# Optimization experiments

Hardware: AMD Instinct MI355X
Metric: run time of the kernel (lower is better)

## Reference

```python
import jax, jax.numpy as jnp
import numpy as np

B, S, D_IN, D_OUT, R = 8, 2048, 4096, 4096, 16

def setup_inputs() -> dict:
    key = jax.random.key(0)
    k = jax.random.split(key, 7)
    return {
        "x": jax.random.normal(k[0], (B, S, D_IN), dtype=jnp.float32),
        "osora_U": jax.random.normal(k[1], (D_OUT, R), dtype=jnp.float32) * 0.02,
        "osora_V": jax.random.normal(k[2], (R, D_IN), dtype=jnp.float32) * 0.02,
        "osora_S": jax.random.normal(k[3], (R,), dtype=jnp.float32),
        "osora_O": jax.random.normal(k[4], (D_OUT,), dtype=jnp.float32),
        "magnitude": jax.random.uniform(k[5], (D_OUT,), dtype=jnp.float32) + 0.5,
        "base_weight": jax.random.normal(k[6], (D_OUT, D_IN), dtype=jnp.float32) * 0.02,
    }

def reference(x, osora_U, osora_V, osora_S, osora_O, magnitude, base_weight):
    # osora_weight = diag(O) @ U @ diag(S) @ V  -> [out, in]
    osora_weight = (osora_O[:, None] * (osora_U * osora_S[None, :])) @ osora_V
    # low-rank path applied to activations: x @ osora_weight.T  -> [B, S, out]
    osora_result = jnp.einsum('bsr,or->bso', jnp.einsum('bsi,ri->bsr', x, osora_V) * osora_S, osora_U) * osora_O
    # weight norm of (base + adapter) per output row; detached in the original
    weight_norm = jax.lax.stop_gradient(
        jnp.linalg.norm(base_weight + osora_weight, axis=1).astype(base_weight.dtype))
    mag_norm_scale = (magnitude / weight_norm)[None, None, :]  # broadcast over B, S
    base_out = jnp.einsum('bsi,oi->bso', x, base_weight)
    return (mag_norm_scale - 1.0) * base_out + mag_norm_scale * osora_result
```

## Files before the change

### kernel.cpp

```cpp
#include <hip/hip_runtime.h>


#define M_TOT 16384
#define N_TOT 4096
#define K_TOT 4096

typedef __attribute__((ext_vector_type(8))) short bf16x8;
typedef __attribute__((ext_vector_type(4))) float f32x4;

__device__ __forceinline__ unsigned short f2bf(float f){
  union { float f; unsigned int u; } v; v.f = f;
  unsigned int u = v.u;
  u += 0x7FFFu + ((u >> 16) & 1u);
  return (unsigned short)(u >> 16);
}

__device__ __forceinline__ void async_lds16(const void* g, void* l){
  __builtin_amdgcn_global_load_lds(
      (const __attribute__((address_space(1))) unsigned int*)g,
      (__attribute__((address_space(3))) unsigned int*)l, 16, 0, 0);
}

__global__ __launch_bounds__(256) void cast_f32_to_bf16_x4(
    const float* __restrict__ src, unsigned short* __restrict__ dst, int n4){
  int i = blockIdx.x * 256 + threadIdx.x;
  if (i >= n4) return;
  float4 v = ((const float4*)src)[i];
  ushort4 o;
  o.x = f2bf(v.x); o.y = f2bf(v.y); o.z = f2bf(v.z); o.w = f2bf(v.w);
  ((ushort4*)dst)[i] = o;
}

__global__ __launch_bounds__(256) void tgemm_kernel(
    const unsigned short* __restrict__ xb, const unsigned short* __restrict__ vb,
    unsigned short* __restrict__ tb){
  int lane = threadIdx.x & 63;
  int wave = threadIdx.x >> 6;
  int quad = lane >> 4;
  int r16  = lane & 15;
  int m0 = (blockIdx.x * 4 + wave) * 16;
  const unsigned short* xptr = xb + (m0 + r16) * K_TOT + quad * 8;
  const unsigned short* vptr = vb + r16 * K_TOT + quad * 8;
  f32x4 acc = {0.f, 0.f, 0.f, 0.f};
  for (int k = 0; k < K_TOT; k += 32){
    bf16x8 a = *(const bf16x8*)(xptr + k);
    bf16x8 b = *(const bf16x8*)(vptr + k);
    acc = __builtin_amdgcn_mfma_f32_16x16x32_bf16(a, b, acc, 0, 0, 0);
  }
  for (int reg = 0; reg < 4; reg++){
    int m = m0 + quad * 4 + reg;
    tb[m * 16 + r16] = f2bf(acc[reg]);
  }
}

__global__ __launch_bounds__(256) void norm_kernel(
    const float* __restrict__ bw, const float* __restrict__ U,
    const float* __restrict__ S, const float* __restrict__ O,
    const float* __restrict__ mag, const float* __restrict__ V,
    float* __restrict__ s_out, float* __restrict__ sm1_out,
    unsigned short* __restrict__ w2b){
  __shared__ float Vl[16 * 1024];
  __shared__ float C8[8 * 16];
  __shared__ float red[8 * 4];
  int t = threadIdx.x;
  int lane = t & 63, wave = t >> 6;
  int n0 = blockIdx.x * 8;
  if (t < 128){
    int row = t >> 4, r = t & 15;
    int n = n0 + row;
    float c = O[n] * S[r] * U[n * 16 + r];
    C8[t] = c;
    w2b[n * 16 + r] = f2bf(c);
  }
  float nsq[8];
  for (int i = 0; i < 8; i++) nsq[i] = 0.f;
  for (int ch = 0; ch < 4; ch++){
    __syncthreads();
    for (int j = 0; j < 16; j++){
      int idx4 = j * 256 + t;
      int r = idx4 >> 8, c4 = idx4 & 255;
      *(float4*)(Vl + r * 1024 + c4 * 4) =
          *(const float4*)(V + r * 4096 + ch * 1024 + c4 * 4);
    }
    __syncthreads();
    for (int row = 0; row < 8; row++){
      float4 b = *(const float4*)(bw + (n0 + row) * 4096 + ch * 1024 + t * 4);
      float a0 = 0.f, a1 = 0.f, a2 = 0.f, a3 = 0.f;
      for (int r = 0; r < 16; r++){
        float cr = C8[row * 16 + r];
        const float* vp = Vl + r * 1024 + t * 4;
        a0 += cr * vp[0]; a1 += cr * vp[1]; a2 += cr * vp[2]; a3 += cr * vp[3];
      }
      float d0 = b.x + a0, d1 = b.y + a1, d2 = b.z + a2, d3 = b.w + a3;
      nsq[row] += d0*d0 + d1*d1 + d2*d2 + d3*d3;
    }
  }
  for (int row = 0; row < 8; row++){
    float v = nsq[row];
    for (int off = 32; off > 0; off >>= 1) v += __shfl_down(v, off);
    if (lane == 0) red[row * 4 + wave] = v;
  }
  __syncthreads();
  if (t < 8){
    int n = n0 + t;
    float tot = red[t*4] + red[t*4+1] + red[t*4+2] + red[t*4+3];
    float s = mag[n] / sqrtf(tot);
    s_out[n] = s;
    sm1_out[n] = s - 1.0f;
  }
}

__global__ __launch_bounds__(512, 2) void gemm_kernel(
    const unsigned short* __restrict__ A,
    const unsigned short* __restrict__ B,
    const unsigned short* __restrict__ Tb,
    const unsigned short* __restrict__ W2b,
    const float* __restrict__ s_arr, const float* __restrict__ sm1_arr,
    float* __restrict__ Cout){
  __shared__ unsigned short AL[2][16384];
  __shared__ unsigned short BL[2][16384];
  int tid  = threadIdx.x;
  int lane = tid & 63;
  int wave = tid >> 6;
  int wm   = wave >> 2;
  int wn   = wave & 3;
  int quad = lane >> 4;
  int r16  = lane & 15;
  int xm   = r16 & 7;

  int bid = blockIdx.x;
  int id  = (bid & 7) * 128 + (bid >> 3);
  int bm = id >> 4, bn = id & 15;
  int m0 = bm * 256, n0 = bn * 256;

  int urow0 = tid >> 3,         uslot0 = tid & 7;
  int urow1 = (512+tid) >> 3,   uslot1 = (512+tid) & 7;
  int ko0 = uslot0 ^ (urow0 & 7);
  int ko1 = uslot1 ^ (urow1 & 7);
  int a_src0 = (m0 + urow0) * K_TOT + ko0 * 8;
  int a_src1 = (m0 + urow1) * K_TOT + ko1 * 8;
  int b_src0 = (n0 + urow0) * K_TOT + ko0 * 8;
  int b_src1 = (n0 + urow1) * K_TOT + ko1 * 8;
  int l_u0 = tid * 8;
  int l_u1 = (512 + tid) * 8;
  const int HSTEP = 128 * K_TOT;

#define STG_A(bf_, h_, kt_) do{ \
    async_lds16(A + a_src0 + (h_)*HSTEP + (kt_)*64, &AL[bf_][(h_)*8192 + l_u0]); \
    async_lds16(A + a_src1 + (h_)*HSTEP + (kt_)*64, &AL[bf_][(h_)*8192 + l_u1]); }while(0)
#define STG_B(bf_, h_, kt_) do{ \
    async_lds16(B + b_src0 + (h_)*HSTEP + (kt_)*64, &BL[bf_][(h_)*8192 + l_u0]); \
    async_lds16(B + b_src1 + (h_)*HSTEP + (kt_)*64, &BL[bf_][(h_)*8192 + l_u1]); }while(0)

#define BARF()  asm volatile("s_barrier" ::: "memory")
#define VMW(n_) asm volatile("s_waitcnt vmcnt(" #n_ ")" ::: "memory")

  int a_row = (wm * 128 + r16) * 64;
  int b_row = (wn * 64  + r16) * 64;
  int koA[2] = { (quad ^ xm) * 8, ((4 + quad) ^ xm) * 8 };

  f32x4 zf = {0.f, 0.f, 0.f, 0.f};
  f32x4 acc[8][4];
#pragma unroll
  for (int i = 0; i < 8; i++)
#pragma unroll
    for (int j = 0; j < 4; j++) acc[i][j] = zf;
  bf16x8 af[4][2], bA[2][2], bB[2][2];

#define RD_A(bf_, mb_) do{ _Pragma("unroll") \
    for (int mf = 0; mf < 4; ++mf){ _Pragma("unroll") \
      for (int ks = 0; ks < 2; ++ks) \
        af[mf][ks] = *(const bf16x8*)(&AL[bf_][a_row + ((mb_)+mf)*1024 + koA[ks]]); } }while(0)
#define RD_B(bf_, dst_, nb_) do{ _Pragma("unroll") \
    for (int nf = 0; nf < 2; ++nf){ _Pragma("unroll") \
      for (int ks = 0; ks < 2; ++ks) \
        dst_[nf][ks] = *(const bf16x8*)(&BL[bf_][b_row + ((nb_)+nf)*1024 + koA[ks]]); } }while(0)
#define MMQ(mb_, bset_, nb_) do{ _Pragma("unroll") \
    for (int ks = 0; ks < 2; ++ks){ _Pragma("unroll") \
      for (int mf = 0; mf < 4; ++mf){ _Pragma("unroll") \
        for (int nf = 0; nf < 2; ++nf) \
          acc[(mb_)+mf][(nb_)+nf] = __builtin_amdgcn_mfma_f32_16x16x32_bf16( \
              af[mf][ks], bset_[nf][ks], acc[(mb_)+mf][(nb_)+nf], 0, 0, 0); } } }while(0)

  STG_A(0, 0, 0); STG_A(0, 1, 0); STG_B(0, 0, 0); STG_B(0, 1, 0);
  STG_B(1, 0, 1); STG_B(1, 1, 1); STG_A(1, 0, 1);
  VMW(6);
  BARF();

#pragma unroll 1
  for (int i = 0; i < 32; ++i){
    int kt = 2 * i;
    int pf = (i < 31);

    RD_A(0, 0); RD_B(0, bA, 0);
    STG_A(1, 1, kt + 1);
    __builtin_amdgcn_s_setprio(1); MMQ(0, bA, 0); __builtin_amdgcn_s_setprio(0);
    BARF();
    RD_B(0, bB, 2);
    __builtin_amdgcn_s_setprio(1); MMQ(0, bB, 2); __builtin_amdgcn_s_setprio(0);
    BARF();
    RD_A(0, 4);
    if (pf) STG_B(0, 0, kt + 2);
    __builtin_amdgcn_s_setprio(1); MMQ(4, bA, 0); __builtin_amdgcn_s_setprio(0);
    BARF();
    if (pf) STG_B(0, 1, kt + 2);
    __builtin_amdgcn_s_setprio(1); MMQ(4, bB, 2); __builtin_amdgcn_s_setprio(0);
    if (pf) { VMW(4); } else { VMW(0); }
    BARF();
    RD_A(1, 0); RD_B(1, bA, 0);
    if (pf) STG_A(0, 0, kt + 2);
    __builtin_amdgcn_s_setprio(1); MMQ(0, bA, 0); __builtin_amdgcn_s_setprio(0);
    BARF();
    RD_B(1, bB, 2);
    if (pf) STG_A(0, 1, kt + 2);
    __builtin_amdgcn_s_setprio(1); MMQ(0, bB, 2); __builtin_amdgcn_s_setprio(0);
    BARF();
    RD_A(1, 4);
    if (pf) STG_B(1, 0, kt + 3);
    __builtin_amdgcn_s_setprio(1); MMQ(4, bA, 0); __builtin_amdgcn_s_setprio(0);
    BARF();
    if (pf) { STG_B(1, 1, kt + 3); STG_A(1, 0, kt + 3); }
    __builtin_amdgcn_s_setprio(1); MMQ(4, bB, 2); __builtin_amdgcn_s_setprio(0);
    VMW(6);
    BARF();
  }

  VMW(0);
  __syncthreads();
  {
    int row = tid >> 1, half = tid & 1;
    uint4 z = {0u, 0u, 0u, 0u};
    unsigned short* Tp = &AL[0][0];
    unsigned short* Wp = &BL[0][0];
    *(uint4*)(Tp + row * 40 + half * 8)      = *(const uint4*)(Tb  + (m0 + row) * 16 + half * 8);
    *(uint4*)(Tp + row * 40 + 16 + half * 8) = z;
    *(uint4*)(Wp + row * 40 + half * 8)      = *(const uint4*)(W2b + (n0 + row) * 16 + half * 8);
    *(uint4*)(Wp + row * 40 + 16 + half * 8) = z;
  }
  __syncthreads();
#pragma unroll
  for (int nf = 0; nf < 4; ++nf){
    int nn = n0 + wn * 64 + nf * 16 + r16;
    float s   = s_arr[nn];
    float sm1 = sm1_arr[nn];
    bf16x8 b2 = *(const bf16x8*)(&BL[0][(wn * 64 + nf * 16 + r16) * 40 + quad * 8]);
#pragma unroll
    for (int mf = 0; mf < 8; ++mf){
      bf16x8 a2 = *(const bf16x8*)(&AL[0][(wm * 128 + mf * 16 + r16) * 40 + quad * 8]);
      f32x4 o2 = __builtin_amdgcn_mfma_f32_16x16x32_bf16(a2, b2, zf, 0, 0, 0);
      int mbase = m0 + wm * 128 + mf * 16 + quad * 4;
      float* cp = Cout + (long)mbase * N_TOT + nn;
      cp[0]         = sm1 * acc[mf][nf][0] + s * o2[0];
      cp[N_TOT]     = sm1 * acc[mf][nf][1] + s * o2[1];
      cp[2 * N_TOT] = sm1 * acc[mf][nf][2] + s * o2[2];
      cp[3 * N_TOT] = sm1 * acc[mf][nf][3] + s * o2[3];
    }
  }
#undef STG_A
#undef STG_B
#undef RD_A
#undef RD_B
#undef MMQ
#undef BARF
#undef VMW
}

extern "C" void kernel_launch(void* const* d_in, const int* in_sizes, int n_in,
                              void* d_out, int out_size, void* d_ws, size_t ws_size,
                              hipStream_t stream){
  const float* x   = (const float*)d_in[0];
  const float* U   = (const float*)d_in[1];
  const float* V   = (const float*)d_in[2];
  const float* S   = (const float*)d_in[3];
  const float* O   = (const float*)d_in[4];
  const float* mag = (const float*)d_in[5];
  const float* bw  = (const float*)d_in[6];
  float* out = (float*)d_out;

  char* ws = (char*)d_ws;
  unsigned short* xb  = (unsigned short*)(ws);
  unsigned short* wb  = (unsigned short*)(ws + 134217728);
  unsigned short* vb  = (unsigned short*)(ws + 167772160);
  unsigned short* tb  = (unsigned short*)(ws + 167903232);
  unsigned short* w2b = (unsigned short*)(ws + 168427520);
  float* s_arr   = (float*)(ws + 168558592);
  float* sm1_arr = (float*)(ws + 168574976);
  (void)in_sizes; (void)n_in; (void)out_size; (void)ws_size;

  cast_f32_to_bf16_x4<<<16384, 256, 0, stream>>>(bw, wb, 4194304);
  cast_f32_to_bf16_x4<<<64,    256, 0, stream>>>(V,  vb, 16384);
  cast_f32_to_bf16_x4<<<65536, 256, 0, stream>>>(x,  xb, 16777216);
  tgemm_kernel<<<256, 256, 0, stream>>>(xb, vb, tb);
  norm_kernel<<<512, 256, 0, stream>>>(bw, U, S, O, mag, V, s_arr, sm1_arr, w2b);
  gemm_kernel<<<1024, 512, 0, stream>>>(xb, wb, tb, w2b, s_arr, sm1_arr, out);
}
```

Measured before the change: 1.046 ms.

## Fuse weight cast into norm kernel, widen cast kernel, software-pipeline LDS reads

Folds the base-weight bf16 cast into the norm kernel, which already reads base_weight, removing one full pass over the weight. The cast kernel now handles four float4 per thread, so far fewer blocks are launched, and the tgemm K loop is unrolled. The main GEMM loop is restructured so A and B fragments for the next half-step are read from LDS earlier, using separate low/high A register sets, with adjusted vmcnt waits. This overlaps LDS reads with MFMA work but raises register pressure and makes the barrier and wait ordering more delicate.

```diff
diff --git a/kernel.cpp b/kernel.cpp
--- a/kernel.cpp
+++ b/kernel.cpp
@@ -21,14 +21,18 @@
       (__attribute__((address_space(3))) unsigned int*)l, 16, 0, 0);
 }
 
-__global__ __launch_bounds__(256) void cast_f32_to_bf16_x4(
+__global__ __launch_bounds__(256) void cast_f32_to_bf16_x16(
     const float* __restrict__ src, unsigned short* __restrict__ dst, int n4){
-  int i = blockIdx.x * 256 + threadIdx.x;
-  if (i >= n4) return;
-  float4 v = ((const float4*)src)[i];
-  ushort4 o;
-  o.x = f2bf(v.x); o.y = f2bf(v.y); o.z = f2bf(v.z); o.w = f2bf(v.w);
-  ((ushort4*)dst)[i] = o;
+  int base = blockIdx.x * 1024 + threadIdx.x;
+#pragma unroll
+  for (int j = 0; j < 4; j++){
+    int i = base + j * 256;
+    if (i >= n4) return;
+    float4 v = ((const float4*)src)[i];
+    ushort4 o;
+    o.x = f2bf(v.x); o.y = f2bf(v.y); o.z = f2bf(v.z); o.w = f2bf(v.w);
+    ((ushort4*)dst)[i] = o;
+  }
 }
 
 __global__ __launch_bounds__(256) void tgemm_kernel(
@@ -42,6 +46,7 @@
   const unsigned short* xptr = xb + (m0 + r16) * K_TOT + quad * 8;
   const unsigned short* vptr = vb + r16 * K_TOT + quad * 8;
   f32x4 acc = {0.f, 0.f, 0.f, 0.f};
+#pragma unroll 4
   for (int k = 0; k < K_TOT; k += 32){
     bf16x8 a = *(const bf16x8*)(xptr + k);
     bf16x8 b = *(const bf16x8*)(vptr + k);
@@ -58,7 +63,7 @@
     const float* __restrict__ S, const float* __restrict__ O,
     const float* __restrict__ mag, const float* __restrict__ V,
     float* __restrict__ s_out, float* __restrict__ sm1_out,
-    unsigned short* __restrict__ w2b){
+    unsigned short* __restrict__ w2b, unsigned short* __restrict__ wb){
   __shared__ float Vl[16 * 1024];
   __shared__ float C8[8 * 16];
   __shared__ float red[8 * 4];
@@ -85,6 +90,9 @@
     __syncthreads();
     for (int row = 0; row < 8; row++){
       float4 b = *(const float4*)(bw + (n0 + row) * 4096 + ch * 1024 + t * 4);
+      ushort4 o;
+      o.x = f2bf(b.x); o.y = f2bf(b.y); o.z = f2bf(b.z); o.w = f2bf(b.w);
+      *(ushort4*)(wb + (n0 + row) * 4096 + ch * 1024 + t * 4) = o;
       float a0 = 0.f, a1 = 0.f, a2 = 0.f, a3 = 0.f;
       for (int r = 0; r < 16; r++){
         float cr = C8[row * 16 + r];
@@ -154,6 +162,8 @@
 
 #define BARF()  asm volatile("s_barrier" ::: "memory")
 #define VMW(n_) asm volatile("s_waitcnt vmcnt(" #n_ ")" ::: "memory")
+#define PRIO1() __builtin_amdgcn_s_setprio(1)
+#define PRIO0() __builtin_amdgcn_s_setprio(0)
 
   int a_row = (wm * 128 + r16) * 64;
   int b_row = (wn * 64  + r16) * 64;
@@ -165,63 +175,71 @@
   for (int i = 0; i < 8; i++)
 #pragma unroll
     for (int j = 0; j < 4; j++) acc[i][j] = zf;
-  bf16x8 af[4][2], bA[2][2], bB[2][2];
-
-#define RD_A(bf_, mb_) do{ _Pragma("unroll") \
+  bf16x8 afL[4][2], afH[4][2], bA[2][2], bB[2][2];
+
+#define RD_AL(bf_) do{ _Pragma("unroll") \
     for (int mf = 0; mf < 4; ++mf){ _Pragma("unroll") \
       for (int ks = 0; ks < 2; ++ks) \
-        af[mf][ks] = *(const bf16x8*)(&AL[bf_][a_row + ((mb_)+mf)*1024 + koA[ks]]); } }while(0)
-#define RD_B(bf_, dst_, nb_) do{ _Pragma("unroll") \
+        afL[mf][ks] = *(const bf16x8*)(&AL[bf_][a_row + mf*1024 + koA[ks]]); } }while(0)
+#define RD_AH(bf_) do{ _Pragma("unroll") \
+    for (int mf = 0; mf < 4; ++mf){ _Pragma("unroll") \
+      for (int ks = 0; ks < 2; ++ks) \
+        afH[mf][ks] = *(const bf16x8*)(&AL[bf_][a_row + (4+mf)*1024 + koA[ks]]); } }while(0)
+#define RD_BA(bf_) do{ _Pragma("unroll") \
     for (int nf = 0; nf < 2; ++nf){ _Pragma("unroll") \
       for (int ks = 0; ks < 2; ++ks) \
-        dst_[nf][ks] = *(const bf16x8*)(&BL[bf_][b_row + ((nb_)+nf)*1024 + koA[ks]]); } }while(0)
-#define MMQ(mb_, bset_, nb_) do{ _Pragma("unroll") \
+        bA[nf][ks] = *(const bf16x8*)(&BL[bf_][b_row + nf*1024 + koA[ks]]); } }while(0)
+#define RD_BB(bf_) do{ _Pragma("unroll") \
+    for (int nf = 0; nf < 2; ++nf){ _Pragma("unroll") \
+      for (int ks = 0; ks < 2; ++ks) \
+        bB[nf][ks] = *(const bf16x8*)(&BL[bf_][b_row + (2+nf)*1024 + koA[ks]]); } }while(0)
+#define MMQ(mb_, afx_, bset_, nb_) do{ _Pragma("unroll") \
     for (int ks = 0; ks < 2; ++ks){ _Pragma("unroll") \
       for (int mf = 0; mf < 4; ++mf){ _Pragma("unroll") \
         for (int nf = 0; nf < 2; ++nf) \
           acc[(mb_)+mf][(nb_)+nf] = __builtin_amdgcn_mfma_f32_16x16x32_bf16( \
-              af[mf][ks], bset_[nf][ks], acc[(mb_)+mf][(nb_)+nf], 0, 0, 0); } } }while(0)
+              afx_[mf][ks], bset_[nf][ks], acc[(mb_)+mf][(nb_)+nf], 0, 0, 0); } } }while(0)
 
   STG_A(0, 0, 0); STG_A(0, 1, 0); STG_B(0, 0, 0); STG_B(0, 1, 0);
   STG_B(1, 0, 1); STG_B(1, 1, 1); STG_A(1, 0, 1);
   VMW(6);
   BARF();
+  RD_AL(0); RD_BA(0);
 
 #pragma unroll 1
   for (int i = 0; i < 32; ++i){
     int kt = 2 * i;
     int pf = (i < 31);
 
-    RD_A(0, 0); RD_B(0, bA, 0);
+    RD_BB(0);
     STG_A(1, 1, kt + 1);
-    __builtin_amdgcn_s_setprio(1); MMQ(0, bA, 0); __builtin_amdgcn_s_setprio(0);
-    BARF();
-    RD_B(0, bB, 2);
-    __builtin_amdgcn_s_setprio(1); MMQ(0, bB, 2); __builtin_amdgcn_s_setprio(0);
-    BARF();
-    RD_A(0, 4);
+    PRIO1(); MMQ(0, afL, bA, 0); PRIO0();
+    BARF();
+    RD_AH(0);
+    PRIO1(); MMQ(0, afL, bB, 2); PRIO0();
+    BARF();
     if (pf) STG_B(0, 0, kt + 2);
-    __builtin_amdgcn_s_setprio(1); MMQ(4, bA, 0); __builtin_amdgcn_s_setprio(0);
-    BARF();
+    PRIO1(); MMQ(4, afH, bA, 0); PRIO0();
+    if (pf) { VMW(2); } else { VMW(0); }
+    BARF();
+    RD_AL(1); RD_BA(1);
     if (pf) STG_B(0, 1, kt + 2);
-    __builtin_amdgcn_s_setprio(1); MMQ(4, bB, 2); __builtin_amdgcn_s_setprio(0);
-    if (pf) { VMW(4); } else { VMW(0); }
-    BARF();
-    RD_A(1, 0); RD_B(1, bA, 0);
+    PRIO1(); MMQ(4, afH, bB, 2); PRIO0();
+    BARF();
+    RD_BB(1);
     if (pf) STG_A(0, 0, kt + 2);
-    __builtin_amdgcn_s_setprio(1); MMQ(0, bA, 0); __builtin_amdgcn_s_setprio(0);
-    BARF();
-    RD_B(1, bB, 2);
+    PRIO1(); MMQ(0, afL, bA, 0); PRIO0();
+    BARF();
+    RD_AH(1);
     if (pf) STG_A(0, 1, kt + 2);
-    __builtin_amdgcn_s_setprio(1); MMQ(0, bB, 2); __builtin_amdgcn_s_setprio(0);
-    BARF();
-    RD_A(1, 4);
+    PRIO1(); MMQ(0, afL, bB, 2); PRIO0();
+    BARF();
     if (pf) STG_B(1, 0, kt + 3);
-    __builtin_amdgcn_s_setprio(1); MMQ(4, bA, 0); __builtin_amdgcn_s_setprio(0);
-    BARF();
-    if (pf) { STG_B(1, 1, kt + 3); STG_A(1, 0, kt + 3); }
-    __builtin_amdgcn_s_setprio(1); MMQ(4, bB, 2); __builtin_amdgcn_s_setprio(0);
-    VMW(6);
+    PRIO1(); MMQ(4, afH, bA, 0); PRIO0();
+    if (pf) { VMW(2); }
+    BARF();
+    if (pf) { RD_AL(0); RD_BA(0); STG_B(1, 1, kt + 3); STG_A(1, 0, kt + 3); }
+    PRIO1(); MMQ(4, afH, bB, 2); PRIO0();
     BARF();
   }
 
@@ -258,11 +276,15 @@
   }
 #undef STG_A
 #undef STG_B
-#undef RD_A
-#undef RD_B
+#undef RD_AL
+#undef RD_AH
+#undef RD_BA
+#undef RD_BB
 #undef MMQ
 #undef BARF
 #undef VMW
+#undef PRIO1
+#undef PRIO0
 }
 
 extern "C" void kernel_launch(void* const* d_in, const int* in_sizes, int n_in,
@@ -287,10 +309,9 @@
   float* sm1_arr = (float*)(ws + 168574976);
   (void)in_sizes; (void)n_in; (void)out_size; (void)ws_size;
 
-  cast_f32_to_bf16_x4<<<16384, 256, 0, stream>>>(bw, wb, 4194304);
-  cast_f32_to_bf16_x4<<<64,    256, 0, stream>>>(V,  vb, 16384);
-  cast_f32_to_bf16_x4<<<65536, 256, 0, stream>>>(x,  xb, 16777216);
+  cast_f32_to_bf16_x16<<<16,    256, 0, stream>>>(V, vb, 16384);
+  cast_f32_to_bf16_x16<<<16384, 256, 0, stream>>>(x, xb, 16777216);
   tgemm_kernel<<<256, 256, 0, stream>>>(xb, vb, tb);
-  norm_kernel<<<512, 256, 0, stream>>>(bw, U, S, O, mag, V, s_arr, sm1_arr, w2b);
+  norm_kernel<<<512, 256, 0, stream>>>(bw, U, S, O, mag, V, s_arr, sm1_arr, w2b, wb);
   gemm_kernel<<<1024, 512, 0, stream>>>(xb, wb, tb, w2b, s_arr, sm1_arr, out);
 }
```

Measured after the change: 1.261 ms. +20.6%, slower.
